# Optimization experiments

Measured on AMD Instinct MI355X. Metric: run time of the kernel, lower is better.

Reference implementation:

```python
import jax, jax.numpy as jnp
import numpy as np
import math

B, T, D, H = 2, 4096, 2048, 16
HD = D // H  # 128
OFFSET = -math.log(math.sqrt(D)) + 1e-6  # q_offset == k_offset in the original


def setup_inputs() -> dict:
    key = jax.random.key(0)
    ks = jax.random.split(key, 7)
    s = 1.0 / np.sqrt(D).astype(np.float32)  # keep exp() in a sane range
    return {
        "hidden_states": jax.random.normal(ks[0], (B, T, D), jnp.float32),
        "Wq": jax.random.normal(ks[1], (D, D), jnp.float32) * s,
        "Wk": jax.random.normal(ks[2], (D, D), jnp.float32) * s,
        "Wv": jax.random.normal(ks[3], (D, D), jnp.float32) * s,
        "Wo": jax.random.normal(ks[4], (D, D), jnp.float32) * s,
        "Fq": jax.random.normal(ks[5], (D, D), jnp.float32) * s,  # q feature map
        "Fk": jax.random.normal(ks[6], (D, D), jnp.float32) * s,  # k feature map
    }


def _split_heads(x):
    # [B, T, D] -> [B, H, T, HD]
    return x.reshape(B, T, H, HD).transpose(0, 2, 1, 3)


def reference(hidden_states, Wq, Wk, Wv, Wo, Fq, Fk):
    q = hidden_states @ Wq
    k = hidden_states @ Wk
    v = hidden_states @ Wv
    # Performer-style positive feature maps
    q_prime = jnp.exp(q @ Fq + OFFSET)
    k_prime = jnp.exp(k @ Fk + OFFSET)
    q_p = _split_heads(q_prime)   # [B,H,T,HD]
    k_p = _split_heads(k_prime)
    v_h = _split_heads(v)
    # causal_attention1: q_t^T (k_t v_t^T) == (q_t . k_t) * v_t, then cumsum over T.
    # Equivalent to the original [B,H,T,HD,HD] outer-product + cumsum, without
    # materializing the huge intermediate.
    dot = jnp.einsum("bhtd,bhtd->bht", q_p, k_p)           # [B,H,T]
    att_raw = jnp.cumsum(dot[..., None] * v_h, axis=2)      # [B,H,T,HD]
    attn = att_raw / k_p                                    # att_norm = k_prime
    # merge heads: [B,H,T,HD] -> [B,T,D]
    attn = attn.transpose(0, 2, 1, 3).reshape(B, T, D)
    return attn @ Wo
```

## Files before the change

kernel.cpp:

```cpp
#include <hip/hip_runtime.h>
#include <hip/hip_bf16.h>
#include <cmath>

constexpr int Bc = 2, Tc = 4096, Dc = 2048, Hc = 16, HDc = 128;
constexpr int Mrows = Bc * Tc;
constexpr int NCHUNK = 32, CHUNK = 128;

__device__ __forceinline__ unsigned short f2bf(float x) {
  union { float f; unsigned int u; } v; v.f = x;
  unsigned int r = v.u + 0x7FFFu + ((v.u >> 16) & 1u);
  return (unsigned short)(r >> 16);
}
__device__ __forceinline__ float bf2f(unsigned short u) {
  union { unsigned int i; float f; } v; v.i = ((unsigned int)u) << 16;
  return v.f;
}

typedef __attribute__((ext_vector_type(8))) short bf16x8;
typedef __attribute__((ext_vector_type(4))) float f32x4;

__device__ __forceinline__ void gload16(const unsigned short* g, unsigned short* l) {
  __builtin_amdgcn_global_load_lds(
      (const __attribute__((address_space(1))) void*)(const void*)g,
      (__attribute__((address_space(3))) void*)(void*)l,
      16, 0, 0);
}

__global__ void cvt_bf16(const float* __restrict__ in, unsigned short* __restrict__ outp) {
  size_t i = ((size_t)blockIdx.x * 256 + threadIdx.x) * 4;
  float4 f = *(const float4*)(in + i);
  ushort4 u;
  u.x = f2bf(f.x); u.y = f2bf(f.y); u.z = f2bf(f.z); u.w = f2bf(f.w);
  *(ushort4*)(outp + i) = u;
}

__global__ void transpose_cvt(const float* __restrict__ W, unsigned short* __restrict__ Wt) {
  __shared__ float tile[32][33];
  int n0 = blockIdx.x * 32, k0 = blockIdx.y * 32;
  int tx = threadIdx.x & 31, ty = threadIdx.x >> 5;
#pragma unroll
  for (int i = 0; i < 4; ++i)
    tile[ty + 8 * i][tx] = W[(size_t)(k0 + ty + 8 * i) * Dc + n0 + tx];
  __syncthreads();
#pragma unroll
  for (int i = 0; i < 4; ++i)
    Wt[(size_t)(n0 + ty + 8 * i) * Dc + k0 + tx] = f2bf(tile[tx][ty + 8 * i]);
}

template <int EPI>
__global__ __launch_bounds__(512, 2) void gemm256(
    const unsigned short* __restrict__ A,
    const unsigned short* __restrict__ Bt,
    void* __restrict__ Cout,
    int M, int N, int lda, int ldc, float eoff) {
  constexpr int K = 2048;
  constexpr int NT = K / 64;
  extern __shared__ unsigned short lds[];

  const int tid = threadIdx.x;
  const int lane = tid & 63;
  const int wave = tid >> 6;
  const int wm = wave >> 2;
  const int wn = wave & 3;

  const int nbn = N >> 8;
  const int nwg = (M >> 8) * nbn;
  const int bidx = (int)blockIdx.x;
  const int wgid = (bidx & 7) * (nwg >> 3) + (bidx >> 3);
  const int bm = wgid / nbn;
  const int bn = wgid % nbn;

  const int srow = tid >> 2;
  const int scolL = (tid & 3) << 3;
  const int scolG = scolL ^ ((srow & 6) << 2);
  const unsigned short* gA = A + (size_t)(bm * 256 + srow) * lda + scolG;
  const unsigned short* gB = Bt + (size_t)(bn * 256 + srow) * K + scolG;
  const int sstage = srow * 32 + scolL;
  const size_t arstep = (size_t)128 * lda;
  const size_t brstep = (size_t)128 * K;

  const int fr = lane & 15;
  const int fko = ((lane >> 4) << 3) ^ ((lane & 6) << 2);
  const int aoff = (wm * 128 + fr) * 32 + fko;
  const int boff = 16384 + (wn * 64 + fr) * 32 + fko;

  f32x4 acc[8][4] = {};
  bf16x8 af[8];
  bf16x8 bfr[2];

  {
    const unsigned short* sA = gA;
    const unsigned short* sB = gB;
    gload16(sA,          lds + sstage);
    gload16(sA + arstep, lds + sstage + 4096);
    gload16(sB,          lds + 16384 + sstage);
    gload16(sB + brstep, lds + 16384 + sstage + 4096);
    gload16(sA + 32,          lds + 8192 + sstage);
    gload16(sA + 32 + arstep, lds + 8192 + sstage + 4096);
    gload16(sB + 32,          lds + 8192 + 16384 + sstage);
    gload16(sB + 32 + brstep, lds + 8192 + 16384 + sstage + 4096);
  }
  asm volatile("s_waitcnt vmcnt(4)" ::: "memory");
  __builtin_amdgcn_s_barrier();

  for (int v = 0; v < NT; ++v) {
    const int b = v & 1;
    const int tn = (v + 1) & (NT - 1);
    const int sb = b * 32768;
    const int db = (b ^ 1) * 32768;
    const unsigned short* srcA = gA + tn * 64;
    const unsigned short* srcB = gB + tn * 64;

    {
#pragma unroll
      for (int mi = 0; mi < 8; ++mi)
        af[mi] = *(const bf16x8*)(lds + sb + aoff + mi * 512);
      bfr[0] = *(const bf16x8*)(lds + sb + boff);
      bfr[1] = *(const bf16x8*)(lds + sb + boff + 512);
      gload16(srcA,          lds + db + sstage);
      gload16(srcA + arstep, lds + db + sstage + 4096);
      __builtin_amdgcn_s_barrier();
      asm volatile("s_waitcnt lgkmcnt(0)" ::: "memory");
      __builtin_amdgcn_s_setprio(1);
#pragma unroll
      for (int mi = 0; mi < 8; ++mi) {
        acc[mi][0] = __builtin_amdgcn_mfma_f32_16x16x32_bf16(af[mi], bfr[0], acc[mi][0], 0, 0, 0);
        acc[mi][1] = __builtin_amdgcn_mfma_f32_16x16x32_bf16(af[mi], bfr[1], acc[mi][1], 0, 0, 0);
      }
      __builtin_amdgcn_s_setprio(0);
      __builtin_amdgcn_s_barrier();
    }
    {
      bfr[0] = *(const bf16x8*)(lds + sb + boff + 1024);
      bfr[1] = *(const bf16x8*)(lds + sb + boff + 1536);
      gload16(srcB,          lds + db + 16384 + sstage);
      gload16(srcB + brstep, lds + db + 16384 + sstage + 4096);
      asm volatile("s_waitcnt vmcnt(4)" ::: "memory");
      __builtin_amdgcn_s_barrier();
      asm volatile("s_waitcnt lgkmcnt(0)" ::: "memory");
      __builtin_amdgcn_s_setprio(1);
#pragma unroll
      for (int mi = 0; mi < 8; ++mi) {
        acc[mi][2] = __builtin_amdgcn_mfma_f32_16x16x32_bf16(af[mi], bfr[0], acc[mi][2], 0, 0, 0);
        acc[mi][3] = __builtin_amdgcn_mfma_f32_16x16x32_bf16(af[mi], bfr[1], acc[mi][3], 0, 0, 0);
      }
      __builtin_amdgcn_s_setprio(0);
      __builtin_amdgcn_s_barrier();
    }
    {
#pragma unroll
      for (int mi = 0; mi < 8; ++mi)
        af[mi] = *(const bf16x8*)(lds + sb + 8192 + aoff + mi * 512);
      bfr[0] = *(const bf16x8*)(lds + sb + 8192 + boff);
      bfr[1] = *(const bf16x8*)(lds + sb + 8192 + boff + 512);
      gload16(srcA + 32,          lds + db + 8192 + sstage);
      gload16(srcA + 32 + arstep, lds + db + 8192 + sstage + 4096);
      __builtin_amdgcn_s_barrier();
      asm volatile("s_waitcnt lgkmcnt(0)" ::: "memory");
      __builtin_amdgcn_s_setprio(1);
#pragma unroll
      for (int mi = 0; mi < 8; ++mi) {
        acc[mi][0] = __builtin_amdgcn_mfma_f32_16x16x32_bf16(af[mi], bfr[0], acc[mi][0], 0, 0, 0);
        acc[mi][1] = __builtin_amdgcn_mfma_f32_16x16x32_bf16(af[mi], bfr[1], acc[mi][1], 0, 0, 0);
      }
      __builtin_amdgcn_s_setprio(0);
      __builtin_amdgcn_s_barrier();
    }
    {
      bfr[0] = *(const bf16x8*)(lds + sb + 8192 + boff + 1024);
      bfr[1] = *(const bf16x8*)(lds + sb + 8192 + boff + 1536);
      gload16(srcB + 32,          lds + db + 8192 + 16384 + sstage);
      gload16(srcB + 32 + brstep, lds + db + 8192 + 16384 + sstage + 4096);
      asm volatile("s_waitcnt vmcnt(4)" ::: "memory");
      __builtin_amdgcn_s_barrier();
      asm volatile("s_waitcnt lgkmcnt(0)" ::: "memory");
      __builtin_amdgcn_s_setprio(1);
#pragma unroll
      for (int mi = 0; mi < 8; ++mi) {
        acc[mi][2] = __builtin_amdgcn_mfma_f32_16x16x32_bf16(af[mi], bfr[0], acc[mi][2], 0, 0, 0);
        acc[mi][3] = __builtin_amdgcn_mfma_f32_16x16x32_bf16(af[mi], bfr[1], acc[mi][3], 0, 0, 0);
      }
      __builtin_amdgcn_s_setprio(0);
      __builtin_amdgcn_s_barrier();
    }
  }

  const int fq = lane >> 4;
  const int crow = bm * 256 + wm * 128;
  const int ccol = bn * 256 + wn * 64 + fr;
#pragma unroll
  for (int mi = 0; mi < 8; ++mi) {
#pragma unroll
    for (int ni = 0; ni < 4; ++ni) {
#pragma unroll
      for (int ii = 0; ii < 4; ++ii) {
        const int r = crow + mi * 16 + fq * 4 + ii;
        const int c = ccol + ni * 16;
        const size_t idx = (size_t)r * ldc + c;
        float vv = acc[mi][ni][ii];
        if (EPI == 0) {
          ((float*)Cout)[idx] = vv;
        } else if (EPI == 1) {
          ((unsigned short*)Cout)[idx] = f2bf(vv);
        } else {
          ((unsigned short*)Cout)[idx] = f2bf(__expf(vv + eoff));
        }
      }
    }
  }
}

__global__ void dot_kernel(const unsigned short* __restrict__ qp,
                           const unsigned short* __restrict__ kp,
                           float* __restrict__ dotb) {
  const int BHT = Bc * Hc * Tc;
  const int lane = threadIdx.x & 63;
  const int qw = lane >> 4;
  const int j = lane & 15;
  const int gw = (blockIdx.x * blockDim.x + threadIdx.x) >> 6;
  const int nw = (gridDim.x * blockDim.x) >> 6;

  for (int flat = gw * 4 + qw; flat < BHT; flat += nw * 4) {
    const int bh = flat >> 12;
    const int t = flat & (Tc - 1);
    const int b = bh >> 4, h = bh & 15;
    const size_t base = ((size_t)(b * Tc + t)) * Dc + h * HDc + j * 8;
    bf16x8 q = *(const bf16x8*)(qp + base);
    bf16x8 k = *(const bf16x8*)(kp + base);
    float p = 0.f;
#pragma unroll
    for (int i = 0; i < 8; ++i)
      p += bf2f((unsigned short)q[i]) * bf2f((unsigned short)k[i]);
#pragma unroll
    for (int m = 8; m; m >>= 1) p += __shfl_xor(p, m);
    if (j == 0) dotb[flat] = p;
  }
}

__global__ void scan_chunks(const float* __restrict__ dotb,
                            const unsigned short* __restrict__ v,
                            float* __restrict__ chks) {
  int bid = blockIdx.x;
  int c = bid % NCHUNK, bh = bid / NCHUNK;
  int b = bh / Hc, h = bh % Hc;
  int d = threadIdx.x;
  const float* dp = dotb + (size_t)bh * Tc + c * CHUNK;
  const unsigned short* vp = v + ((size_t)(b * Tc + c * CHUNK)) * Dc + h * HDc + d;
  float acc = 0.f;
  for (int t = 0; t < CHUNK; ++t)
    acc += dp[t] * bf2f(vp[(size_t)t * Dc]);
  chks[(size_t)bid * HDc + d] = acc;
}

__global__ void scan_offsets(float* __restrict__ chks) {
  int bh = blockIdx.x;
  int d = threadIdx.x;
  float run = 0.f;
  for (int c = 0; c < NCHUNK; ++c) {
    size_t idx = ((size_t)bh * NCHUNK + c) * HDc + d;
    float tmp = chks[idx];
    chks[idx] = run;
    run += tmp;
  }
}

__global__ void scan_final(const float* __restrict__ dotb,
                           const unsigned short* __restrict__ v,
                           const unsigned short* __restrict__ kp,
                           const float* __restrict__ chks,
                           unsigned short* __restrict__ attn) {
  int bid = blockIdx.x;
  int c = bid % NCHUNK, bh = bid / NCHUNK;
  int b = bh / Hc, h = bh % Hc;
  int d = threadIdx.x;
  const float* dp = dotb + (size_t)bh * Tc + c * CHUNK;
  size_t base = ((size_t)(b * Tc + c * CHUNK)) * Dc + h * HDc + d;
  float acc = chks[(size_t)bid * HDc + d];
  for (int t = 0; t < CHUNK; ++t) {
    size_t idx = base + (size_t)t * Dc;
    acc += dp[t] * bf2f(v[idx]);
    attn[idx] = f2bf(acc / bf2f(kp[idx]));
  }
}

extern "C" void kernel_launch(void* const* d_in, const int* in_sizes, int n_in,
                              void* d_out, int out_size, void* d_ws, size_t ws_size,
                              hipStream_t stream) {
  const float* hs = (const float*)d_in[0];
  const float* Wq = (const float*)d_in[1];
  const float* Wk = (const float*)d_in[2];
  const float* Wv = (const float*)d_in[3];
  const float* Wo = (const float*)d_in[4];
  const float* Fq = (const float*)d_in[5];
  const float* Fk = (const float*)d_in[6];
  float* out = (float*)d_out;

  const size_t MD = (size_t)Mrows * Dc;
  const size_t DD = (size_t)Dc * Dc;

  char* w = (char*)d_ws;
  size_t off = 0;
  auto take = [&](size_t bytes) -> void* {
    void* r = w + off;
    off += (bytes + 255) & ~(size_t)255;
    return r;
  };

  unsigned short* hs_bf = (unsigned short*)take(MD * 2);
  unsigned short* wtq  = (unsigned short*)take(DD * 2);
  unsigned short* wtk  = (unsigned short*)take(DD * 2);
  unsigned short* wtv  = (unsigned short*)take(DD * 2);
  unsigned short* wto  = (unsigned short*)take(DD * 2);
  unsigned short* wtfq = (unsigned short*)take(DD * 2);
  unsigned short* wtfk = (unsigned short*)take(DD * 2);
  unsigned short* Qbf  = (unsigned short*)take(MD * 2);
  unsigned short* Kbf  = (unsigned short*)take(MD * 2);
  unsigned short* Vbf  = (unsigned short*)take(MD * 2);
  float* dotb = (float*)take((size_t)Bc * Hc * Tc * 4);
  float* chks = (float*)take((size_t)Bc * Hc * NCHUNK * HDc * 4);

  unsigned short* Qp = hs_bf;
  unsigned short* Kp = Qbf;
  unsigned short* attnbf = Kbf;

  const float OFF = (float)(-0.5 * log(2048.0) + 1e-6);

  (void)hipFuncSetAttribute((const void*)gemm256<0>, hipFuncAttributeMaxDynamicSharedMemorySize, 131072);
  (void)hipFuncSetAttribute((const void*)gemm256<1>, hipFuncAttributeMaxDynamicSharedMemorySize, 131072);
  (void)hipFuncSetAttribute((const void*)gemm256<2>, hipFuncAttributeMaxDynamicSharedMemorySize, 131072);

  cvt_bf16<<<(int)(MD / 1024), 256, 0, stream>>>(hs, hs_bf);

  dim3 tg(Dc / 32, Dc / 32);
  transpose_cvt<<<tg, 256, 0, stream>>>(Wq, wtq);
  transpose_cvt<<<tg, 256, 0, stream>>>(Wk, wtk);
  transpose_cvt<<<tg, 256, 0, stream>>>(Wv, wtv);
  transpose_cvt<<<tg, 256, 0, stream>>>(Wo, wto);
  transpose_cvt<<<tg, 256, 0, stream>>>(Fq, wtfq);
  transpose_cvt<<<tg, 256, 0, stream>>>(Fk, wtfk);

  const int gblocks = (Mrows / 256) * (Dc / 256);

  gemm256<1><<<gblocks, 512, 131072, stream>>>(hs_bf, wtq, Qbf, Mrows, Dc, Dc, Dc, 0.f);
  gemm256<1><<<gblocks, 512, 131072, stream>>>(hs_bf, wtk, Kbf, Mrows, Dc, Dc, Dc, 0.f);
  gemm256<1><<<gblocks, 512, 131072, stream>>>(hs_bf, wtv, Vbf, Mrows, Dc, Dc, Dc, 0.f);

  gemm256<2><<<gblocks, 512, 131072, stream>>>(Qbf, wtfq, Qp, Mrows, Dc, Dc, Dc, OFF);
  gemm256<2><<<gblocks, 512, 131072, stream>>>(Kbf, wtfk, Kp, Mrows, Dc, Dc, Dc, OFF);

  dot_kernel<<<1024, 256, 0, stream>>>(Qp, Kp, dotb);

  scan_chunks<<<Bc * Hc * NCHUNK, 128, 0, stream>>>(dotb, Vbf, chks);
  scan_offsets<<<Bc * Hc, 128, 0, stream>>>(chks);
  scan_final<<<Bc * Hc * NCHUNK, 128, 0, stream>>>(dotb, Vbf, Kp, chks, attnbf);

  gemm256<0><<<gblocks, 512, 131072, stream>>>(attnbf, wto, out, Mrows, Dc, Dc, Dc, 0.f);
}
```

Before: 522.1 us.

## Precompose Wq·Fq and Wk·Fk weights and fuse QKV into one wide GEMM

Multiplies the weight matrices together up front (Wq@Fq and Wk@Fk) in a small new paired GEMM kernel. This turns the two-stage q and k feature-map projections over the large activation matrix into a single projection. The three projections (q', k', v) then run as one 6144-wide GEMM whose epilogue applies exp only to the q/k segments and routes each output to its own buffer. This removes two full Mrows×D×D GEMMs and several launches, at the cost of a D×D×D weight GEMM plus extra bf16 rounding of the combined weights, which changes numerics.

```diff
diff --git a/kernel.cpp b/kernel.cpp
--- a/kernel.cpp
+++ b/kernel.cpp
@@ -47,11 +47,85 @@
     Wt[(size_t)(n0 + ty + 8 * i) * Dc + k0 + tx] = f2bf(tile[tx][ty + 8 * i]);
 }
 
+__global__ __launch_bounds__(256) void gemm_pair(
+    const unsigned short* __restrict__ A0, const unsigned short* __restrict__ B0,
+    unsigned short* __restrict__ C0,
+    const unsigned short* __restrict__ A1, const unsigned short* __restrict__ B1,
+    unsigned short* __restrict__ C1) {
+  constexpr int K = 2048, N = 2048;
+  constexpr int BK = 32;
+  __shared__ __align__(16) unsigned short lds_a[128 * BK];
+  __shared__ __align__(16) unsigned short lds_b[128 * BK];
+
+  const unsigned short* A = blockIdx.y ? A1 : A0;
+  const unsigned short* Bt = blockIdx.y ? B1 : B0;
+  unsigned short* C = blockIdx.y ? C1 : C0;
+
+  const int tid = threadIdx.x;
+  const int wave = tid >> 6;
+  const int lane = tid & 63;
+
+  const int nbn = N / 128;
+  const int nwg = (2048 / 128) * nbn;
+  const int bid = blockIdx.x;
+  const int wgid = (bid & 7) * (nwg >> 3) + (bid >> 3);
+  const int bm = wgid / nbn;
+  const int bn = wgid % nbn;
+
+  const int wm = wave >> 1, wn = wave & 1;
+  const int srow = tid >> 2;
+  const int scolL = (tid & 3) << 3;
+  const int scolG = scolL ^ ((srow & 6) << 2);
+
+  const unsigned short* ga = A + (size_t)(bm * 128 + srow) * K + scolG;
+  const unsigned short* gb = Bt + (size_t)(bn * 128 + srow) * K + scolG;
+  const size_t rstep = (size_t)64 * K;
+
+  f32x4 acc[4][4] = {};
+
+  const int fr = lane & 15;
+  const int fko = ((lane >> 4) << 3) ^ ((lane & 6) << 2);
+
+  for (int kt = 0; kt < K; kt += BK) {
+    gload16(ga,         lds_a + wave * 512);
+    gload16(ga + rstep, lds_a + 2048 + wave * 512);
+    gload16(gb,         lds_b + wave * 512);
+    gload16(gb + rstep, lds_b + 2048 + wave * 512);
+    ga += BK; gb += BK;
+    __syncthreads();
+
+    bf16x8 af[4], bfr[4];
+#pragma unroll
+    for (int i = 0; i < 4; ++i) {
+      af[i]  = *(const bf16x8*)(lds_a + (wm * 64 + i * 16 + fr) * BK + fko);
+      bfr[i] = *(const bf16x8*)(lds_b + (wn * 64 + i * 16 + fr) * BK + fko);
+    }
+#pragma unroll
+    for (int mi = 0; mi < 4; ++mi)
+#pragma unroll
+      for (int ni = 0; ni < 4; ++ni)
+        acc[mi][ni] = __builtin_amdgcn_mfma_f32_16x16x32_bf16(af[mi], bfr[ni], acc[mi][ni], 0, 0, 0);
+    __syncthreads();
+  }
+
+  const int fq = lane >> 4;
+#pragma unroll
+  for (int mi = 0; mi < 4; ++mi)
+#pragma unroll
+    for (int ni = 0; ni < 4; ++ni)
+#pragma unroll
+      for (int ii = 0; ii < 4; ++ii) {
+        const int row = bm * 128 + wm * 64 + mi * 16 + fq * 4 + ii;
+        const int col = bn * 128 + wn * 64 + ni * 16 + fr;
+        C[(size_t)row * N + col] = f2bf(acc[mi][ni][ii]);
+      }
+}
+
 template <int EPI>
 __global__ __launch_bounds__(512, 2) void gemm256(
     const unsigned short* __restrict__ A,
     const unsigned short* __restrict__ Bt,
-    void* __restrict__ Cout,
+    void* __restrict__ Cout, void* __restrict__ C1, void* __restrict__ C2,
     int M, int N, int lda, int ldc, float eoff) {
   constexpr int K = 2048;
   constexpr int NT = K / 64;
@@ -187,26 +261,42 @@
 
   const int fq = lane >> 4;
   const int crow = bm * 256 + wm * 128;
-  const int ccol = bn * 256 + wn * 64 + fr;
-#pragma unroll
-  for (int mi = 0; mi < 8; ++mi) {
-#pragma unroll
-    for (int ni = 0; ni < 4; ++ni) {
-#pragma unroll
-      for (int ii = 0; ii < 4; ++ii) {
-        const int r = crow + mi * 16 + fq * 4 + ii;
-        const int c = ccol + ni * 16;
-        const size_t idx = (size_t)r * ldc + c;
-        float vv = acc[mi][ni][ii];
-        if (EPI == 0) {
-          ((float*)Cout)[idx] = vv;
-        } else if (EPI == 1) {
-          ((unsigned short*)Cout)[idx] = f2bf(vv);
-        } else {
-          ((unsigned short*)Cout)[idx] = f2bf(__expf(vv + eoff));
+  if (EPI == 3) {
+    const int seg = bn >> 3;
+    unsigned short* outp = (unsigned short*)(seg == 0 ? Cout : (seg == 1 ? C1 : C2));
+    const int ccol = (bn & 7) * 256 + wn * 64 + fr;
+#pragma unroll
+    for (int mi = 0; mi < 8; ++mi)
+#pragma unroll
+      for (int ni = 0; ni < 4; ++ni)
+#pragma unroll
+        for (int ii = 0; ii < 4; ++ii) {
+          const int r = crow + mi * 16 + fq * 4 + ii;
+          const int c = ccol + ni * 16;
+          float vv = acc[mi][ni][ii];
+          if (seg < 2) vv = __expf(vv + eoff);
+          outp[(size_t)r * ldc + c] = f2bf(vv);
         }
-      }
-    }
+  } else {
+    const int ccol = bn * 256 + wn * 64 + fr;
+#pragma unroll
+    for (int mi = 0; mi < 8; ++mi)
+#pragma unroll
+      for (int ni = 0; ni < 4; ++ni)
+#pragma unroll
+        for (int ii = 0; ii < 4; ++ii) {
+          const int r = crow + mi * 16 + fq * 4 + ii;
+          const int c = ccol + ni * 16;
+          const size_t idx = (size_t)r * ldc + c;
+          float vv = acc[mi][ni][ii];
+          if (EPI == 0) {
+            ((float*)Cout)[idx] = vv;
+          } else if (EPI == 1) {
+            ((unsigned short*)Cout)[idx] = f2bf(vv);
+          } else {
+            ((unsigned short*)Cout)[idx] = f2bf(__expf(vv + eoff));
+          }
+        }
   }
 }
 
@@ -307,46 +397,41 @@
   };
 
   unsigned short* hs_bf = (unsigned short*)take(MD * 2);
-  unsigned short* wtq  = (unsigned short*)take(DD * 2);
-  unsigned short* wtk  = (unsigned short*)take(DD * 2);
-  unsigned short* wtv  = (unsigned short*)take(DD * 2);
-  unsigned short* wto  = (unsigned short*)take(DD * 2);
-  unsigned short* wtfq = (unsigned short*)take(DD * 2);
-  unsigned short* wtfk = (unsigned short*)take(DD * 2);
-  unsigned short* Qbf  = (unsigned short*)take(MD * 2);
-  unsigned short* Kbf  = (unsigned short*)take(MD * 2);
-  unsigned short* Vbf  = (unsigned short*)take(MD * 2);
+  unsigned short* wq_bf = (unsigned short*)take(DD * 2);
+  unsigned short* wtfq  = (unsigned short*)take(DD * 2);
+  unsigned short* wk_bf = (unsigned short*)take(DD * 2);
+  unsigned short* wtfk  = (unsigned short*)take(DD * 2);
+  unsigned short* wcat  = (unsigned short*)take(3 * DD * 2);
+  unsigned short* wto   = (unsigned short*)take(DD * 2);
+  unsigned short* Kp    = (unsigned short*)take(MD * 2);
+  unsigned short* Vbf   = (unsigned short*)take(MD * 2);
   float* dotb = (float*)take((size_t)Bc * Hc * Tc * 4);
   float* chks = (float*)take((size_t)Bc * Hc * NCHUNK * HDc * 4);
 
-  unsigned short* Qp = hs_bf;
-  unsigned short* Kp = Qbf;
-  unsigned short* attnbf = Kbf;
+  unsigned short* Qp = wq_bf;
+  unsigned short* attnbf = hs_bf;
 
   const float OFF = (float)(-0.5 * log(2048.0) + 1e-6);
 
   (void)hipFuncSetAttribute((const void*)gemm256<0>, hipFuncAttributeMaxDynamicSharedMemorySize, 131072);
-  (void)hipFuncSetAttribute((const void*)gemm256<1>, hipFuncAttributeMaxDynamicSharedMemorySize, 131072);
-  (void)hipFuncSetAttribute((const void*)gemm256<2>, hipFuncAttributeMaxDynamicSharedMemorySize, 131072);
+  (void)hipFuncSetAttribute((const void*)gemm256<3>, hipFuncAttributeMaxDynamicSharedMemorySize, 131072);
 
   cvt_bf16<<<(int)(MD / 1024), 256, 0, stream>>>(hs, hs_bf);
+  cvt_bf16<<<(int)(DD / 1024), 256, 0, stream>>>(Wq, wq_bf);
+  cvt_bf16<<<(int)(DD / 1024), 256, 0, stream>>>(Wk, wk_bf);
 
   dim3 tg(Dc / 32, Dc / 32);
-  transpose_cvt<<<tg, 256, 0, stream>>>(Wq, wtq);
-  transpose_cvt<<<tg, 256, 0, stream>>>(Wk, wtk);
-  transpose_cvt<<<tg, 256, 0, stream>>>(Wv, wtv);
-  transpose_cvt<<<tg, 256, 0, stream>>>(Wo, wto);
   transpose_cvt<<<tg, 256, 0, stream>>>(Fq, wtfq);
   transpose_cvt<<<tg, 256, 0, stream>>>(Fk, wtfk);
-
-  const int gblocks = (Mrows / 256) * (Dc / 256);
-
-  gemm256<1><<<gblocks, 512, 131072, stream>>>(hs_bf, wtq, Qbf, Mrows, Dc, Dc, Dc, 0.f);
-  gemm256<1><<<gblocks, 512, 131072, stream>>>(hs_bf, wtk, Kbf, Mrows, Dc, Dc, Dc, 0.f);
-  gemm256<1><<<gblocks, 512, 131072, stream>>>(hs_bf, wtv, Vbf, Mrows, Dc, Dc, Dc, 0.f);
-
-  gemm256<2><<<gblocks, 512, 131072, stream>>>(Qbf, wtfq, Qp, Mrows, Dc, Dc, Dc, OFF);
-  gemm256<2><<<gblocks, 512, 131072, stream>>>(Kbf, wtfk, Kp, Mrows, Dc, Dc, Dc, OFF);
+  transpose_cvt<<<tg, 256, 0, stream>>>(Wv, wcat + 2 * DD);
+  transpose_cvt<<<tg, 256, 0, stream>>>(Wo, wto);
+
+  gemm_pair<<<dim3(256, 2), 256, 0, stream>>>(wtfq, wq_bf, wcat,
+                                              wtfk, wk_bf, wcat + DD);
+
+  const int fblocks = (Mrows / 256) * (6144 / 256);
+  gemm256<3><<<fblocks, 512, 131072, stream>>>(hs_bf, wcat, Qp, Kp, Vbf,
+                                               Mrows, 6144, Dc, Dc, OFF);
 
   dot_kernel<<<1024, 256, 0, stream>>>(Qp, Kp, dotb);
 
@@ -354,5 +439,7 @@
   scan_offsets<<<Bc * Hc, 128, 0, stream>>>(chks);
   scan_final<<<Bc * Hc * NCHUNK, 128, 0, stream>>>(dotb, Vbf, Kp, chks, attnbf);
 
-  gemm256<0><<<gblocks, 512, 131072, stream>>>(attnbf, wto, out, Mrows, Dc, Dc, Dc, 0.f);
-}
+  const int gblocks = (Mrows / 256) * (Dc / 256);
+  gemm256<0><<<gblocks, 512, 131072, stream>>>(attnbf, wto, out, nullptr, nullptr,
+                                               Mrows, Dc, Dc, Dc, 0.f);
+}
```

After: 444.4 us. -14.9%, faster.

## Precompose Wq·Fq and Wk·Fk weights and fuse projections into one wide GEMM

Applied to the files above, without the earlier changes.

Uses associativity to precompute (Wq·Fq)^T and (Wk·Fk)^T as small 2048x2048 weight GEMMs, so the two chained activation GEMMs collapse into one. The Q', K' and V projections then run as a single 6144-wide GEMM that applies the exp epilogue per output segment. The GEMM kernel is also rewritten with K-step 32 and a 4-stage LDS ring in place of double buffering. This removes two full M×D×D activation GEMMs and the Q/K intermediates, at the cost of bf16 rounding of the composed weights, which changes numerics slightly before the exp.

```diff
diff --git a/kernel.cpp b/kernel.cpp
--- a/kernel.cpp
+++ b/kernel.cpp
@@ -47,24 +47,38 @@
     Wt[(size_t)(n0 + ty + 8 * i) * Dc + k0 + tx] = f2bf(tile[tx][ty + 8 * i]);
 }
 
-template <int EPI>
-__global__ __launch_bounds__(512, 2) void gemm256(
-    const unsigned short* __restrict__ A,
-    const unsigned short* __restrict__ Bt,
-    void* __restrict__ Cout,
+template <int EPI, int WMw, int WNw, int MI, int NI>
+__global__ __launch_bounds__(WMw * WNw * 64, 2) void gemmP(
+    const unsigned short* __restrict__ A0, const unsigned short* __restrict__ B0,
+    void* __restrict__ C0, void* __restrict__ C1, void* __restrict__ C2,
+    const unsigned short* __restrict__ A1, const unsigned short* __restrict__ B1,
+    void* __restrict__ C1a,
     int M, int N, int lda, int ldc, float eoff) {
   constexpr int K = 2048;
-  constexpr int NT = K / 64;
+  constexpr int NT = K / 32;
+  constexpr int THREADS = WMw * WNw * 64;
+  constexpr int BM = WMw * MI * 16;
+  constexpr int BN = WNw * NI * 16;
+  constexpr int ASLAB = BM * 32;
+  constexpr int BSLAB = BN * 32;
+  constexpr int BUF = ASLAB + BSLAB;
+  constexpr int SROWS = THREADS / 4;
+  static_assert(2 * SROWS == BM && BM == BN, "staging geometry");
   extern __shared__ unsigned short lds[];
+
+  const unsigned short* A = A0;
+  const unsigned short* Bt = B0;
+  void* Cz = C0;
+  if (blockIdx.y) { A = A1; Bt = B1; Cz = C1a; }
 
   const int tid = threadIdx.x;
   const int lane = tid & 63;
   const int wave = tid >> 6;
-  const int wm = wave >> 2;
-  const int wn = wave & 3;
-
-  const int nbn = N >> 8;
-  const int nwg = (M >> 8) * nbn;
+  const int wm = wave / WNw;
+  const int wn = wave % WNw;
+
+  const int nbn = N / BN;
+  const int nwg = (M / BM) * nbn;
   const int bidx = (int)blockIdx.x;
   const int wgid = (bidx & 7) * (nwg >> 3) + (bidx >> 3);
   const int bm = wgid / nbn;
@@ -73,140 +87,114 @@
   const int srow = tid >> 2;
   const int scolL = (tid & 3) << 3;
   const int scolG = scolL ^ ((srow & 6) << 2);
-  const unsigned short* gA = A + (size_t)(bm * 256 + srow) * lda + scolG;
-  const unsigned short* gB = Bt + (size_t)(bn * 256 + srow) * K + scolG;
+  const unsigned short* gA = A + (size_t)(bm * BM + srow) * lda + scolG;
+  const unsigned short* gB = Bt + (size_t)(bn * BN + srow) * K + scolG;
   const int sstage = srow * 32 + scolL;
-  const size_t arstep = (size_t)128 * lda;
-  const size_t brstep = (size_t)128 * K;
+  const size_t arstep = (size_t)SROWS * lda;
+  const size_t brstep = (size_t)SROWS * K;
 
   const int fr = lane & 15;
   const int fko = ((lane >> 4) << 3) ^ ((lane & 6) << 2);
-  const int aoff = (wm * 128 + fr) * 32 + fko;
-  const int boff = 16384 + (wn * 64 + fr) * 32 + fko;
-
-  f32x4 acc[8][4] = {};
-  bf16x8 af[8];
-  bf16x8 bfr[2];
-
-  {
-    const unsigned short* sA = gA;
-    const unsigned short* sB = gB;
-    gload16(sA,          lds + sstage);
-    gload16(sA + arstep, lds + sstage + 4096);
-    gload16(sB,          lds + 16384 + sstage);
-    gload16(sB + brstep, lds + 16384 + sstage + 4096);
-    gload16(sA + 32,          lds + 8192 + sstage);
-    gload16(sA + 32 + arstep, lds + 8192 + sstage + 4096);
-    gload16(sB + 32,          lds + 8192 + 16384 + sstage);
-    gload16(sB + 32 + brstep, lds + 8192 + 16384 + sstage + 4096);
-  }
-  asm volatile("s_waitcnt vmcnt(4)" ::: "memory");
+  const int aoff = (wm * MI * 16 + fr) * 32 + fko;
+  const int boff = ASLAB + (wn * NI * 16 + fr) * 32 + fko;
+
+  f32x4 acc[MI][NI] = {};
+  bf16x8 afr[MI / 2];
+  bf16x8 bfr[NI];
+
+#pragma unroll
+  for (int t = 0; t < 3; ++t) {
+    const unsigned short* sA = gA + t * 32;
+    const unsigned short* sB = gB + t * 32;
+    unsigned short* dst = lds + t * BUF;
+    gload16(sA,          dst + sstage);
+    gload16(sA + arstep, dst + sstage + SROWS * 32);
+    gload16(sB,          dst + ASLAB + sstage);
+    gload16(sB + brstep, dst + ASLAB + sstage + SROWS * 32);
+  }
+  asm volatile("s_waitcnt vmcnt(8)" ::: "memory");
   __builtin_amdgcn_s_barrier();
 
   for (int v = 0; v < NT; ++v) {
-    const int b = v & 1;
-    const int tn = (v + 1) & (NT - 1);
-    const int sb = b * 32768;
-    const int db = (b ^ 1) * 32768;
-    const unsigned short* srcA = gA + tn * 64;
-    const unsigned short* srcB = gB + tn * 64;
+    const int rb = (v & 3) * BUF;
+    const int wb = ((v + 3) & 3) * BUF;
+    const int tn = (v + 3) & (NT - 1);
+    const unsigned short* srcA = gA + tn * 32;
+    const unsigned short* srcB = gB + tn * 32;
 
     {
 #pragma unroll
-      for (int mi = 0; mi < 8; ++mi)
-        af[mi] = *(const bf16x8*)(lds + sb + aoff + mi * 512);
-      bfr[0] = *(const bf16x8*)(lds + sb + boff);
-      bfr[1] = *(const bf16x8*)(lds + sb + boff + 512);
-      gload16(srcA,          lds + db + sstage);
-      gload16(srcA + arstep, lds + db + sstage + 4096);
+      for (int mi = 0; mi < MI / 2; ++mi)
+        afr[mi] = *(const bf16x8*)(lds + rb + aoff + mi * 512);
+#pragma unroll
+      for (int ni = 0; ni < NI; ++ni)
+        bfr[ni] = *(const bf16x8*)(lds + rb + boff + ni * 512);
+      gload16(srcA,          lds + wb + sstage);
+      gload16(srcA + arstep, lds + wb + sstage + SROWS * 32);
       __builtin_amdgcn_s_barrier();
       asm volatile("s_waitcnt lgkmcnt(0)" ::: "memory");
       __builtin_amdgcn_s_setprio(1);
 #pragma unroll
-      for (int mi = 0; mi < 8; ++mi) {
-        acc[mi][0] = __builtin_amdgcn_mfma_f32_16x16x32_bf16(af[mi], bfr[0], acc[mi][0], 0, 0, 0);
-        acc[mi][1] = __builtin_amdgcn_mfma_f32_16x16x32_bf16(af[mi], bfr[1], acc[mi][1], 0, 0, 0);
-      }
+      for (int mi = 0; mi < MI / 2; ++mi)
+#pragma unroll
+        for (int ni = 0; ni < NI; ++ni)
+          acc[mi][ni] = __builtin_amdgcn_mfma_f32_16x16x32_bf16(afr[mi], bfr[ni], acc[mi][ni], 0, 0, 0);
       __builtin_amdgcn_s_setprio(0);
       __builtin_amdgcn_s_barrier();
     }
     {
-      bfr[0] = *(const bf16x8*)(lds + sb + boff + 1024);
-      bfr[1] = *(const bf16x8*)(lds + sb + boff + 1536);
-      gload16(srcB,          lds + db + 16384 + sstage);
-      gload16(srcB + brstep, lds + db + 16384 + sstage + 4096);
-      asm volatile("s_waitcnt vmcnt(4)" ::: "memory");
+#pragma unroll
+      for (int mi = 0; mi < MI / 2; ++mi)
+        afr[mi] = *(const bf16x8*)(lds + rb + aoff + (MI / 2 + mi) * 512);
+      gload16(srcB,          lds + wb + ASLAB + sstage);
+      gload16(srcB + brstep, lds + wb + ASLAB + sstage + SROWS * 32);
+      asm volatile("s_waitcnt vmcnt(8)" ::: "memory");
       __builtin_amdgcn_s_barrier();
       asm volatile("s_waitcnt lgkmcnt(0)" ::: "memory");
       __builtin_amdgcn_s_setprio(1);
 #pragma unroll
-      for (int mi = 0; mi < 8; ++mi) {
-        acc[mi][2] = __builtin_amdgcn_mfma_f32_16x16x32_bf16(af[mi], bfr[0], acc[mi][2], 0, 0, 0);
-        acc[mi][3] = __builtin_amdgcn_mfma_f32_16x16x32_bf16(af[mi], bfr[1], acc[mi][3], 0, 0, 0);
-      }
+      for (int mi = 0; mi < MI / 2; ++mi)
+#pragma unroll
+        for (int ni = 0; ni < NI; ++ni)
+          acc[MI / 2 + mi][ni] = __builtin_amdgcn_mfma_f32_16x16x32_bf16(afr[mi], bfr[ni], acc[MI / 2 + mi][ni], 0, 0, 0);
       __builtin_amdgcn_s_setprio(0);
       __builtin_amdgcn_s_barrier();
     }
-    {
-#pragma unroll
-      for (int mi = 0; mi < 8; ++mi)
-        af[mi] = *(const bf16x8*)(lds + sb + 8192 + aoff + mi * 512);
-      bfr[0] = *(const bf16x8*)(lds + sb + 8192 + boff);
-      bfr[1] = *(const bf16x8*)(lds + sb + 8192 + boff + 512);
-      gload16(srcA + 32,          lds + db + 8192 + sstage);
-      gload16(srcA + 32 + arstep, lds + db + 8192 + sstage + 4096);
-      __builtin_amdgcn_s_barrier();
-      asm volatile("s_waitcnt lgkmcnt(0)" ::: "memory");
-      __builtin_amdgcn_s_setprio(1);
-#pragma unroll
-      for (int mi = 0; mi < 8; ++mi) {
-        acc[mi][0] = __builtin_amdgcn_mfma_f32_16x16x32_bf16(af[mi], bfr[0], acc[mi][0], 0, 0, 0);
-        acc[mi][1] = __builtin_amdgcn_mfma_f32_16x16x32_bf16(af[mi], bfr[1], acc[mi][1], 0, 0, 0);
-      }
-      __builtin_amdgcn_s_setprio(0);
-      __builtin_amdgcn_s_barrier();
-    }
-    {
-      bfr[0] = *(const bf16x8*)(lds + sb + 8192 + boff + 1024);
-      bfr[1] = *(const bf16x8*)(lds + sb + 8192 + boff + 1536);
-      gload16(srcB + 32,          lds + db + 8192 + 16384 + sstage);
-      gload16(srcB + 32 + brstep, lds + db + 8192 + 16384 + sstage + 4096);
-      asm volatile("s_waitcnt vmcnt(4)" ::: "memory");
-      __builtin_amdgcn_s_barrier();
-      asm volatile("s_waitcnt lgkmcnt(0)" ::: "memory");
-      __builtin_amdgcn_s_setprio(1);
-#pragma unroll
-      for (int mi = 0; mi < 8; ++mi) {
-        acc[mi][2] = __builtin_amdgcn_mfma_f32_16x16x32_bf16(af[mi], bfr[0], acc[mi][2], 0, 0, 0);
-        acc[mi][3] = __builtin_amdgcn_mfma_f32_16x16x32_bf16(af[mi], bfr[1], acc[mi][3], 0, 0, 0);
-      }
-      __builtin_amdgcn_s_setprio(0);
-      __builtin_amdgcn_s_barrier();
-    }
   }
 
   const int fq = lane >> 4;
-  const int crow = bm * 256 + wm * 128;
-  const int ccol = bn * 256 + wn * 64 + fr;
-#pragma unroll
-  for (int mi = 0; mi < 8; ++mi) {
-#pragma unroll
-    for (int ni = 0; ni < 4; ++ni) {
-#pragma unroll
-      for (int ii = 0; ii < 4; ++ii) {
-        const int r = crow + mi * 16 + fq * 4 + ii;
-        const int c = ccol + ni * 16;
-        const size_t idx = (size_t)r * ldc + c;
-        float vv = acc[mi][ni][ii];
-        if (EPI == 0) {
-          ((float*)Cout)[idx] = vv;
-        } else if (EPI == 1) {
-          ((unsigned short*)Cout)[idx] = f2bf(vv);
-        } else {
-          ((unsigned short*)Cout)[idx] = f2bf(__expf(vv + eoff));
+  const int crow = bm * BM + wm * (MI * 16);
+  if constexpr (EPI == 3) {
+    const int seg = bn >> 3;
+    unsigned short* outp = (unsigned short*)(seg == 0 ? C0 : (seg == 1 ? C1 : C2));
+    const int ccol = (bn & 7) * BN + wn * (NI * 16) + fr;
+#pragma unroll
+    for (int mi = 0; mi < MI; ++mi)
+#pragma unroll
+      for (int ni = 0; ni < NI; ++ni)
+#pragma unroll
+        for (int ii = 0; ii < 4; ++ii) {
+          const int r = crow + mi * 16 + fq * 4 + ii;
+          const int c = ccol + ni * 16;
+          float vv = acc[mi][ni][ii];
+          if (seg < 2) vv = __expf(vv + eoff);
+          outp[(size_t)r * ldc + c] = f2bf(vv);
         }
-      }
-    }
+  } else {
+    const int ccol = bn * BN + wn * (NI * 16) + fr;
+#pragma unroll
+    for (int mi = 0; mi < MI; ++mi)
+#pragma unroll
+      for (int ni = 0; ni < NI; ++ni)
+#pragma unroll
+        for (int ii = 0; ii < 4; ++ii) {
+          const int r = crow + mi * 16 + fq * 4 + ii;
+          const int c = ccol + ni * 16;
+          const size_t idx = (size_t)r * ldc + c;
+          float vv = acc[mi][ni][ii];
+          if (EPI == 0) ((float*)Cz)[idx] = vv;
+          else          ((unsigned short*)Cz)[idx] = f2bf(vv);
+        }
   }
 }
 
@@ -307,46 +295,45 @@
   };
 
   unsigned short* hs_bf = (unsigned short*)take(MD * 2);
-  unsigned short* wtq  = (unsigned short*)take(DD * 2);
-  unsigned short* wtk  = (unsigned short*)take(DD * 2);
-  unsigned short* wtv  = (unsigned short*)take(DD * 2);
-  unsigned short* wto  = (unsigned short*)take(DD * 2);
-  unsigned short* wtfq = (unsigned short*)take(DD * 2);
-  unsigned short* wtfk = (unsigned short*)take(DD * 2);
-  unsigned short* Qbf  = (unsigned short*)take(MD * 2);
-  unsigned short* Kbf  = (unsigned short*)take(MD * 2);
-  unsigned short* Vbf  = (unsigned short*)take(MD * 2);
+  unsigned short* wq_bf = (unsigned short*)take(DD * 2);
+  unsigned short* wtfq  = (unsigned short*)take(DD * 2);
+  unsigned short* wk_bf = (unsigned short*)take(DD * 2);
+  unsigned short* wtfk  = (unsigned short*)take(DD * 2);
+  unsigned short* wcat  = (unsigned short*)take(3 * DD * 2);
+  unsigned short* wto   = (unsigned short*)take(DD * 2);
+  unsigned short* Kp    = (unsigned short*)take(MD * 2);
+  unsigned short* Vbf   = (unsigned short*)take(MD * 2);
   float* dotb = (float*)take((size_t)Bc * Hc * Tc * 4);
   float* chks = (float*)take((size_t)Bc * Hc * NCHUNK * HDc * 4);
 
-  unsigned short* Qp = hs_bf;
-  unsigned short* Kp = Qbf;
-  unsigned short* attnbf = Kbf;
+  unsigned short* Qp = wq_bf;
+  unsigned short* attnbf = hs_bf;
 
   const float OFF = (float)(-0.5 * log(2048.0) + 1e-6);
 
-  (void)hipFuncSetAttribute((const void*)gemm256<0>, hipFuncAttributeMaxDynamicSharedMemorySize, 131072);
-  (void)hipFuncSetAttribute((const void*)gemm256<1>, hipFuncAttributeMaxDynamicSharedMemorySize, 131072);
-  (void)hipFuncSetAttribute((const void*)gemm256<2>, hipFuncAttributeMaxDynamicSharedMemorySize, 131072);
+  (void)hipFuncSetAttribute((const void*)gemmP<0, 2, 4, 8, 4>, hipFuncAttributeMaxDynamicSharedMemorySize, 131072);
+  (void)hipFuncSetAttribute((const void*)gemmP<3, 2, 4, 8, 4>, hipFuncAttributeMaxDynamicSharedMemorySize, 131072);
+  (void)hipFuncSetAttribute((const void*)gemmP<1, 2, 2, 4, 4>, hipFuncAttributeMaxDynamicSharedMemorySize, 65536);
 
   cvt_bf16<<<(int)(MD / 1024), 256, 0, stream>>>(hs, hs_bf);
+  cvt_bf16<<<(int)(DD / 1024), 256, 0, stream>>>(Wq, wq_bf);
+  cvt_bf16<<<(int)(DD / 1024), 256, 0, stream>>>(Wk, wk_bf);
 
   dim3 tg(Dc / 32, Dc / 32);
-  transpose_cvt<<<tg, 256, 0, stream>>>(Wq, wtq);
-  transpose_cvt<<<tg, 256, 0, stream>>>(Wk, wtk);
-  transpose_cvt<<<tg, 256, 0, stream>>>(Wv, wtv);
-  transpose_cvt<<<tg, 256, 0, stream>>>(Wo, wto);
   transpose_cvt<<<tg, 256, 0, stream>>>(Fq, wtfq);
   transpose_cvt<<<tg, 256, 0, stream>>>(Fk, wtfk);
-
-  const int gblocks = (Mrows / 256) * (Dc / 256);
-
-  gemm256<1><<<gblocks, 512, 131072, stream>>>(hs_bf, wtq, Qbf, Mrows, Dc, Dc, Dc, 0.f);
-  gemm256<1><<<gblocks, 512, 131072, stream>>>(hs_bf, wtk, Kbf, Mrows, Dc, Dc, Dc, 0.f);
-  gemm256<1><<<gblocks, 512, 131072, stream>>>(hs_bf, wtv, Vbf, Mrows, Dc, Dc, Dc, 0.f);
-
-  gemm256<2><<<gblocks, 512, 131072, stream>>>(Qbf, wtfq, Qp, Mrows, Dc, Dc, Dc, OFF);
-  gemm256<2><<<gblocks, 512, 131072, stream>>>(Kbf, wtfk, Kp, Mrows, Dc, Dc, Dc, OFF);
+  transpose_cvt<<<tg, 256, 0, stream>>>(Wv, wcat + 2 * DD);
+  transpose_cvt<<<tg, 256, 0, stream>>>(Wo, wto);
+
+  gemmP<1, 2, 2, 4, 4><<<dim3(256, 2), 256, 65536, stream>>>(
+      wtfq, wq_bf, wcat, nullptr, nullptr,
+      wtfk, wk_bf, wcat + DD,
+      2048, 2048, 2048, 2048, 0.f);
+
+  const int fblocks = (Mrows / 256) * (6144 / 256);
+  gemmP<3, 2, 4, 8, 4><<<fblocks, 512, 131072, stream>>>(
+      hs_bf, wcat, Qp, Kp, Vbf, nullptr, nullptr, nullptr,
+      Mrows, 6144, Dc, Dc, OFF);
 
   dot_kernel<<<1024, 256, 0, stream>>>(Qp, Kp, dotb);
 
@@ -354,5 +341,8 @@
   scan_offsets<<<Bc * Hc, 128, 0, stream>>>(chks);
   scan_final<<<Bc * Hc * NCHUNK, 128, 0, stream>>>(dotb, Vbf, Kp, chks, attnbf);
 
-  gemm256<0><<<gblocks, 512, 131072, stream>>>(attnbf, wto, out, Mrows, Dc, Dc, Dc, 0.f);
-}
+  const int gblocks = (Mrows / 256) * (Dc / 256);
+  gemmP<0, 2, 4, 8, 4><<<gblocks, 512, 131072, stream>>>(
+      attnbf, wto, out, nullptr, nullptr, nullptr, nullptr, nullptr,
+      Mrows, Dc, Dc, Dc, 0.f);
+}
```

Result: faster. 443.9 us (-15.0%).
